# Kernel tuning notes

Measured on AMD Instinct MI355X. Metric: run time of the kernel, lower is better.

The kernel has to match this reference:

```python
import jax, jax.numpy as jnp
import numpy as np

N = 100000   # nodes
E = 1600000  # directed edges
F_IN = 256
H = 128
C = 64

def setup_inputs() -> dict:
    key = jax.random.key(0)
    k = jax.random.split(key, 6)
    x = jax.random.normal(k[0], (N, F_IN), dtype=jnp.float32)
    edge_index = jax.random.randint(k[1], (2, E), 0, N)
    def glorot(kk, fan_in, fan_out):
        s = jnp.sqrt(6.0 / (fan_in + fan_out)).astype(jnp.float32)
        return jax.random.uniform(kk, (fan_in, fan_out), jnp.float32, -s, s)
    W0 = glorot(k[2], F_IN, H)
    W1 = glorot(k[3], H, H)
    W2 = glorot(k[4], H, H)
    W3 = glorot(k[5], H, C)
    return {"x": x, "edge_index": edge_index, "W0": W0, "W1": W1, "W2": W2, "W3": W3}

def _gcn_norm(edge_index, num_nodes):
    # add self loops, compute symmetric normalization 1/sqrt(deg_i * deg_j)
    loops = jnp.arange(num_nodes, dtype=edge_index.dtype)
    row = jnp.concatenate([edge_index[0], loops])
    col = jnp.concatenate([edge_index[1], loops])
    deg = jax.ops.segment_sum(jnp.ones_like(row, dtype=jnp.float32), row, num_segments=num_nodes)
    dinv = jnp.where(deg > 0, jax.lax.rsqrt(deg), 0.0)
    norm = dinv[row] * dinv[col]  # [E+N]
    return row, col, norm

def _gcn_conv(h, W, row, col, norm, num_nodes):
    h = h @ W                      # [N, d_out]
    msg = h[col] * norm[:, None]   # gather + scale, [E+N, d_out]
    return jax.ops.segment_sum(msg, row, num_segments=num_nodes)

def _feat_corr_metric(h):
    # torch_corr(x.t()): Pearson correlation across feature columns -> [d, d]
    hc = h - jnp.mean(h, axis=0, keepdims=True)
    cov = hc.T @ hc                                 # [d, d]
    sd = jnp.sqrt(jnp.clip(jnp.diag(cov), 1e-12))
    corr = cov / (sd[:, None] * sd[None, :])
    n = corr.shape[0]
    upper = jnp.abs(jnp.triu(corr, 1))
    return upper.sum() / (n * (n - 1) / 2)

def reference(x, edge_index, W0, W1, W2, W3):
    row, col, norm = _gcn_norm(edge_index, N)
    Ws = [W0, W1, W2, W3]
    num_layers = len(Ws)
    h = x
    corr_2 = jnp.float32(0.0)
    corr = jnp.float32(0.0)
    for i, W in enumerate(Ws):
        h = _gcn_conv(h, W, row, col, norm, N)  # type_norm='None' -> bn is identity; eval -> dropout identity
        if i == num_layers - 2:
            corr_2 = _feat_corr_metric(h)
        if i == num_layers - 1:
            corr = _feat_corr_metric(h)
        if i != num_layers - 1:
            h = jax.nn.relu(h)
    return h, corr_2, corr
```

## Files before the change

kernel.cpp:

```cpp
#include <hip/hip_runtime.h>

#define NN 100000
#define FIN 256
#define HD 128
#define CD 64

typedef __attribute__((ext_vector_type(8))) short bf16x8;
typedef __attribute__((ext_vector_type(4))) float f32x4;

__device__ __forceinline__ float bf2f(unsigned int u16) {
    union { unsigned int u; float f; } v;
    v.u = (u16 & 0xffffu) << 16;
    return v.f;
}
__device__ __forceinline__ unsigned short f2bf(float f) {
    union { float f; unsigned int u; } v;
    v.f = f;
    unsigned int u = v.u + 0x7fffu + ((v.u >> 16) & 1u);
    return (unsigned short)(u >> 16);
}

__global__ void k_detect(const unsigned short* __restrict__ x, int* __restrict__ flag) {
    __shared__ int s[256];
    int t = threadIdx.x;
    int c = 0;
    for (int i = t; i < 16384; i += 256) {
        unsigned int e = (x[2 * i] >> 7) & 0xFF;
        c += (e >= 112 && e <= 134) ? 1 : 0;
    }
    s[t] = c;
    __syncthreads();
    for (int off = 128; off > 0; off >>= 1) {
        if (t < off) s[t] += s[t + off];
        __syncthreads();
    }
    if (t == 0) *flag = (s[0] > 8192) ? 1 : 0;
}

template <int K, int COLS>
__global__ void k_packW(const void* __restrict__ src, unsigned short* __restrict__ dst,
                        const int* __restrict__ dflag) {
    constexpr int CT = COLS / 16;
    int i = blockIdx.x * 256 + threadIdx.x;
    if (i >= K * COLS) return;
    int j = i & 7;
    int lane = (i >> 3) & 63;
    int rest = i >> 9;
    int ct = rest % CT;
    int kt = rest / CT;
    int k = kt * 32 + (lane >> 4) * 8 + j;
    int c = ct * 16 + (lane & 15);
    int si = k * COLS + c;
    dst[i] = (*dflag) ? ((const unsigned short*)src)[si] : f2bf(((const float*)src)[si]);
}

__global__ void k_hist(const int* __restrict__ row, int* __restrict__ cnt, int E) {
    int e = blockIdx.x * 256 + threadIdx.x;
    if (e < E) {
        unsigned int r = (unsigned int)row[e];
        if (r >= NN) r = 0;
        atomicAdd(&cnt[r], 1);
    }
}

__global__ void k_scan_a(const int* __restrict__ cnt, int* __restrict__ bsum, int n) {
    __shared__ int s[256];
    int i = blockIdx.x * 256 + threadIdx.x;
    s[threadIdx.x] = (i < n) ? cnt[i] : 0;
    __syncthreads();
    for (int off = 128; off > 0; off >>= 1) {
        if (threadIdx.x < off) s[threadIdx.x] += s[threadIdx.x + off];
        __syncthreads();
    }
    if (threadIdx.x == 0) bsum[blockIdx.x] = s[0];
}

__global__ void k_scan_b(int* bsum, int nchunks) {
    __shared__ int s[512];
    int t = threadIdx.x;
    int v = (t < nchunks) ? bsum[t] : 0;
    s[t] = v;
    __syncthreads();
    for (int off = 1; off < 512; off <<= 1) {
        int x = (t >= off) ? s[t - off] : 0;
        __syncthreads();
        s[t] += x;
        __syncthreads();
    }
    if (t < nchunks) bsum[t] = s[t] - v;
}

__global__ void k_scan_c(const int* __restrict__ cnt, const int* __restrict__ bsum,
                         int* __restrict__ offs, int* __restrict__ cursor, int n) {
    __shared__ int s[256];
    int t = threadIdx.x;
    int i = blockIdx.x * 256 + t;
    int v = (i < n) ? cnt[i] : 0;
    s[t] = v;
    __syncthreads();
    for (int off = 1; off < 256; off <<= 1) {
        int x = (t >= off) ? s[t - off] : 0;
        __syncthreads();
        s[t] += x;
        __syncthreads();
    }
    if (i < n) {
        int ex = bsum[blockIdx.x] + s[t] - v;
        offs[i] = ex;
        cursor[i] = ex;
    }
}

__global__ void k_scatter(const int* __restrict__ row, const int* __restrict__ col,
                          int* __restrict__ cursor, int* __restrict__ colS, int E,
                          int lo, int hi) {
    int e = blockIdx.x * 256 + threadIdx.x;
    if (e < E) {
        unsigned int r = (unsigned int)row[e];
        if (r >= NN) r = 0;
        if ((int)r >= lo && (int)r < hi) {
            unsigned int c = (unsigned int)col[e];
            if (c >= NN) c = 0;
            int p = atomicAdd(&cursor[r], 1);
            colS[p] = (int)c;
        }
    }
}

__global__ void k_dinv(const int* __restrict__ cnt, float* __restrict__ dinv, int n) {
    int i = blockIdx.x * 256 + threadIdx.x;
    if (i < n) dinv[i] = rsqrtf((float)(cnt[i] + 1));
}

template <int K, int COLS, bool RELU, int AMODE>
__global__ __launch_bounds__(256) void k_gemm(const void* __restrict__ Av,
                                              const unsigned short* __restrict__ Wp,
                                              const float* __restrict__ dinv,
                                              unsigned short* __restrict__ G, int nrows,
                                              const int* __restrict__ dflag) {
    constexpr int CT = COLS / 16;
    constexpr int KT = K / 32;
    __shared__ unsigned short tile[4][16][136];

    int t = threadIdx.x;
    int wave = t >> 6, lane = t & 63;
    int quad = lane >> 4, m = lane & 15;
    int r0 = blockIdx.x * 64 + wave * 16;
    int arow = r0 + m;
    bool rowok = arow < nrows;
    bool abf = (AMODE == 0) || (*dflag != 0);

    const unsigned short* Ab = (const unsigned short*)Av;
    const float* Af = (const float*)Av;

    f32x4 acc[CT];
#pragma unroll
    for (int ct = 0; ct < CT; ct++) acc[ct] = (f32x4){0.f, 0.f, 0.f, 0.f};

    for (int kt = 0; kt < KT; kt++) {
        int kb = kt * 32 + quad * 8;
        bf16x8 afrag = (bf16x8)0;
        if (rowok) {
            if (abf) {
                afrag = *(const bf16x8*)(Ab + (size_t)arow * K + kb);
                if constexpr (RELU) {
#pragma unroll
                    for (int j = 0; j < 8; j++) {
                        unsigned short u = (unsigned short)afrag[j];
                        afrag[j] = (u & 0x8000u) ? (short)0 : (short)u;
                    }
                }
            } else {
                float4 f0 = *(const float4*)(Af + (size_t)arow * K + kb);
                float4 f1 = *(const float4*)(Af + (size_t)arow * K + kb + 4);
                afrag[0] = (short)f2bf(f0.x); afrag[1] = (short)f2bf(f0.y);
                afrag[2] = (short)f2bf(f0.z); afrag[3] = (short)f2bf(f0.w);
                afrag[4] = (short)f2bf(f1.x); afrag[5] = (short)f2bf(f1.y);
                afrag[6] = (short)f2bf(f1.z); afrag[7] = (short)f2bf(f1.w);
            }
        }
#pragma unroll
        for (int ct = 0; ct < CT; ct++) {
            bf16x8 bfrag = *(const bf16x8*)(Wp + (((size_t)kt * CT + ct) * 64 + lane) * 8);
            acc[ct] = __builtin_amdgcn_mfma_f32_16x16x32_bf16(afrag, bfrag, acc[ct], 0, 0, 0);
        }
    }

    float dv[4];
#pragma unroll
    for (int rg = 0; rg < 4; rg++) {
        int gr = r0 + quad * 4 + rg;
        dv[rg] = dinv[gr < nrows ? gr : 0];
    }
#pragma unroll
    for (int ct = 0; ct < CT; ct++) {
#pragma unroll
        for (int rg = 0; rg < 4; rg++)
            tile[wave][quad * 4 + rg][ct * 16 + m] = f2bf(acc[ct][rg] * dv[rg]);
    }
    int srow = lane >> 2;
    int grow = r0 + srow;
    if (grow < nrows) {
        constexpr int CH = COLS / 32;
#pragma unroll
        for (int j8 = 0; j8 < CH; j8++) {
            int c = (lane & 3) * 8 + j8 * 32;
            uint4 v = *(const uint4*)&tile[wave][srow][c];
            *(uint4*)(G + (size_t)grow * COLS + c) = v;
        }
    }
}

template <int D, bool RELU, bool FINAL>
__global__ __launch_bounds__(256) void k_agg(const unsigned short* __restrict__ g,
                                             const int* __restrict__ colS,
                                             const int* __restrict__ offs,
                                             const int* __restrict__ cnt,
                                             const float* __restrict__ dinv,
                                             unsigned short* __restrict__ obf,
                                             void* __restrict__ oraw,
                                             const int* __restrict__ dflag, int n) {
    int lane = threadIdx.x & 63;
    int node = blockIdx.x * 4 + (threadIdx.x >> 6);
    if (node >= n) return;
    int start = offs[node];
    int deg = cnt[node];

    float a0 = 0.f, a1 = 0.f;
    if constexpr (D == 128) {
        unsigned int u = *(const unsigned int*)(g + (size_t)node * 128 + lane * 2);
        a0 = bf2f(u); a1 = bf2f(u >> 16);
    } else {
        a0 = bf2f(g[(size_t)node * 64 + lane]);
    }

    for (int base = 0; base < deg; base += 64) {
        int rem = deg - base;
        int nb = rem < 64 ? rem : 64;
        int cidx = 0;
        if (lane < nb) cidx = colS[start + base + lane];
        int j = 0;
        for (; j + 8 <= nb; j += 8) {
            int c0 = __shfl(cidx, j);
            int c1 = __shfl(cidx, j + 1);
            int c2 = __shfl(cidx, j + 2);
            int c3 = __shfl(cidx, j + 3);
            int c4 = __shfl(cidx, j + 4);
            int c5 = __shfl(cidx, j + 5);
            int c6 = __shfl(cidx, j + 6);
            int c7 = __shfl(cidx, j + 7);
            if constexpr (D == 128) {
                unsigned int u0 = *(const unsigned int*)(g + (size_t)c0 * 128 + lane * 2);
                unsigned int u1 = *(const unsigned int*)(g + (size_t)c1 * 128 + lane * 2);
                unsigned int u2 = *(const unsigned int*)(g + (size_t)c2 * 128 + lane * 2);
                unsigned int u3 = *(const unsigned int*)(g + (size_t)c3 * 128 + lane * 2);
                unsigned int u4 = *(const unsigned int*)(g + (size_t)c4 * 128 + lane * 2);
                unsigned int u5 = *(const unsigned int*)(g + (size_t)c5 * 128 + lane * 2);
                unsigned int u6 = *(const unsigned int*)(g + (size_t)c6 * 128 + lane * 2);
                unsigned int u7 = *(const unsigned int*)(g + (size_t)c7 * 128 + lane * 2);
                a0 += bf2f(u0); a1 += bf2f(u0 >> 16);
                a0 += bf2f(u1); a1 += bf2f(u1 >> 16);
                a0 += bf2f(u2); a1 += bf2f(u2 >> 16);
                a0 += bf2f(u3); a1 += bf2f(u3 >> 16);
                a0 += bf2f(u4); a1 += bf2f(u4 >> 16);
                a0 += bf2f(u5); a1 += bf2f(u5 >> 16);
                a0 += bf2f(u6); a1 += bf2f(u6 >> 16);
                a0 += bf2f(u7); a1 += bf2f(u7 >> 16);
            } else {
                unsigned short u0 = g[(size_t)c0 * 64 + lane];
                unsigned short u1 = g[(size_t)c1 * 64 + lane];
                unsigned short u2 = g[(size_t)c2 * 64 + lane];
                unsigned short u3 = g[(size_t)c3 * 64 + lane];
                unsigned short u4 = g[(size_t)c4 * 64 + lane];
                unsigned short u5 = g[(size_t)c5 * 64 + lane];
                unsigned short u6 = g[(size_t)c6 * 64 + lane];
                unsigned short u7 = g[(size_t)c7 * 64 + lane];
                a0 += bf2f(u0) + bf2f(u1) + bf2f(u2) + bf2f(u3);
                a0 += bf2f(u4) + bf2f(u5) + bf2f(u6) + bf2f(u7);
            }
        }
        for (; j < nb; j++) {
            int cj = __shfl(cidx, j);
            if constexpr (D == 128) {
                unsigned int u = *(const unsigned int*)(g + (size_t)cj * 128 + lane * 2);
                a0 += bf2f(u); a1 += bf2f(u >> 16);
            } else {
                a0 += bf2f(g[(size_t)cj * 64 + lane]);
            }
        }
    }

    float s = dinv[node];
    a0 *= s; a1 *= s;
    if constexpr (RELU) { a0 = fmaxf(a0, 0.f); a1 = fmaxf(a1, 0.f); }

    if constexpr (D == 128) {
        *(unsigned int*)(obf + (size_t)node * 128 + lane * 2) =
            (unsigned int)f2bf(a0) | ((unsigned int)f2bf(a1) << 16);
    } else {
        obf[(size_t)node * 64 + lane] = f2bf(a0);
        if constexpr (FINAL) {
            if (*dflag) ((unsigned short*)oraw)[(size_t)node * 64 + lane] = f2bf(a0);
            else        ((float*)oraw)[(size_t)node * 64 + lane] = a0;
        }
    }
}

template <int D>
__global__ __launch_bounds__(256) void k_colsum(const unsigned short* __restrict__ in,
                                                float* __restrict__ colsum, int n) {
    constexpr int CG = D / 8;
    constexpr int RPB = 256 / CG;
    __shared__ float red[RPB][D];
    int t = threadIdx.x;
    int cg = t % CG, r0 = t / CG;
    int c0 = cg * 8;
    float a[8];
#pragma unroll
    for (int i = 0; i < 8; i++) a[i] = 0.f;
    for (int r = blockIdx.x * RPB + r0; r < n; r += gridDim.x * RPB) {
        bf16x8 u = *(const bf16x8*)(in + (size_t)r * D + c0);
#pragma unroll
        for (int i = 0; i < 8; i++) a[i] += bf2f((unsigned short)u[i]);
    }
#pragma unroll
    for (int i = 0; i < 8; i++) red[r0][c0 + i] = a[i];
    __syncthreads();
    if (t < D) {
        float s = 0.f;
#pragma unroll
        for (int r = 0; r < RPB; r++) s += red[r][t];
        atomicAdd(&colsum[t], s);
    }
}

template <int D>
__global__ __launch_bounds__(256) void k_cov2(const unsigned short* __restrict__ in,
                                              const float* __restrict__ colsum,
                                              float* __restrict__ part, int n, int nblocks) {
    constexpr int CT = D / 16;
    constexpr int TPW = (D == 128) ? 2 : 1;
    constexpr int CG = D / 8;
    __shared__ unsigned int lds32[D * 16];
    __shared__ float smean[D];

    int t = threadIdx.x;
    int wave = t >> 6, lane = t & 63;
    int quad = lane >> 4, m = lane & 15;

    if (t < D) smean[t] = colsum[t] * (1.0f / (float)NN);
    __syncthreads();

    f32x4 accA[CT], accB[CT];
#pragma unroll
    for (int tc = 0; tc < CT; tc++) {
        accA[tc] = (f32x4){0.f, 0.f, 0.f, 0.f};
        accB[tc] = (f32x4){0.f, 0.f, 0.f, 0.f};
    }

    bool stager = (t < 16 * CG);
    int kp = stager ? (t / CG) : 0;
    int c0 = stager ? ((t % CG) * 8) : 0;
    int slot = (((kp >> 2) + (c0 >> 3)) & 3) * 4 + (kp & 3);
    float sm[8];
#pragma unroll
    for (int i = 0; i < 8; i++) sm[i] = smean[c0 + i];

    int ca0 = (wave * TPW) * 16 + m;
    int ga0 = (quad + (ca0 >> 3)) & 3;
    int ca1 = ca0 + 16;
    int ga1 = (quad + (ca1 >> 3)) & 3;

    int nchunks = (n + 31) / 32;
    for (int ch = blockIdx.x; ch < nchunks; ch += nblocks) {
        int k0 = ch * 32;
        if (stager) {
            int k = k0 + 2 * kp;
            bf16x8 u0 = (bf16x8)0, u1 = (bf16x8)0;
            bool ok0 = (k < n), ok1 = (k + 1 < n);
            if (ok0) u0 = *(const bf16x8*)(in + (size_t)k * D + c0);
            if (ok1) u1 = *(const bf16x8*)(in + (size_t)(k + 1) * D + c0);
#pragma unroll
            for (int i = 0; i < 8; i++) {
                float a = ok0 ? (bf2f((unsigned short)u0[i]) - sm[i]) : 0.f;
                float b = ok1 ? (bf2f((unsigned short)u1[i]) - sm[i]) : 0.f;
                lds32[(c0 + i) * 16 + slot] = (unsigned int)f2bf(a) | ((unsigned int)f2bf(b) << 16);
            }
        }
        __syncthreads();

        bf16x8 bfr[CT];
#pragma unroll
        for (int tc = 0; tc < CT; tc++) {
            int c = tc * 16 + m;
            int grp = (quad + (c >> 3)) & 3;
            bfr[tc] = *(const bf16x8*)&lds32[c * 16 + grp * 4];
        }
        bf16x8 afr0 = *(const bf16x8*)&lds32[ca0 * 16 + ga0 * 4];
#pragma unroll
        for (int tc = 0; tc < CT; tc++)
            accA[tc] = __builtin_amdgcn_mfma_f32_16x16x32_bf16(afr0, bfr[tc], accA[tc], 0, 0, 0);
        if constexpr (TPW == 2) {
            bf16x8 afr1 = *(const bf16x8*)&lds32[ca1 * 16 + ga1 * 4];
#pragma unroll
            for (int tc = 0; tc < CT; tc++)
                accB[tc] = __builtin_amdgcn_mfma_f32_16x16x32_bf16(afr1, bfr[tc], accB[tc], 0, 0, 0);
        }
        __syncthreads();
    }

    float* p = part + (size_t)blockIdx.x * D * D;
    int tr0 = wave * TPW;
#pragma unroll
    for (int tc = 0; tc < CT; tc++) {
#pragma unroll
        for (int rg = 0; rg < 4; rg++) {
            int cj = tc * 16 + m;
            p[(tr0 * 16 + quad * 4 + rg) * D + cj] = accA[tc][rg];
            if constexpr (TPW == 2)
                p[((tr0 + 1) * 16 + quad * 4 + rg) * D + cj] = accB[tc][rg];
        }
    }
}

template <int D>
__global__ __launch_bounds__(256) void k_covred(const float* __restrict__ part,
                                                float* __restrict__ cov, int nblocks) {
    __shared__ float red[256];
    int t = threadIdx.x;
    int il = t & 63;
    int bs = t >> 6;
    int idx = blockIdx.x * 64 + il;
    float s = 0.f;
    for (int b = bs; b < nblocks; b += 4)
        s += part[(size_t)b * D * D + idx];
    red[t] = s;
    __syncthreads();
    if (t < 64)
        cov[idx] = red[t] + red[t + 64] + red[t + 128] + red[t + 192];
}

template <int D>
__global__ __launch_bounds__(256) void k_fin(const float* __restrict__ cov,
                                             void* __restrict__ out, long long idx,
                                             const int* __restrict__ dflag) {
    __shared__ float sd[D];
    __shared__ float red[256];
    int t = threadIdx.x;
    if (t < D) sd[t] = sqrtf(fmaxf(cov[t * D + t], 1e-12f));
    __syncthreads();
    float s = 0.f;
    for (int i2 = t; i2 < D * D; i2 += 256) {
        int i = i2 / D, j = i2 % D;
        if (j > i) s += fabsf(cov[i2] / (sd[i] * sd[j]));
    }
    red[t] = s;
    __syncthreads();
    for (int off = 128; off > 0; off >>= 1) {
        if (t < off) red[t] += red[t + off];
        __syncthreads();
    }
    if (t == 0) {
        float v = red[0] / (float)(D * (D - 1) / 2);
        if (*dflag) ((unsigned short*)out)[idx] = f2bf(v);
        else        ((float*)out)[idx] = v;
    }
}

extern "C" void kernel_launch(void* const* d_in, const int* in_sizes, int n_in,
                              void* d_out, int out_size, void* d_ws, size_t ws_size,
                              hipStream_t stream) {
    const void* x = d_in[0];
    const int* ei = (const int*)d_in[1];

    int E = in_sizes[1] / 2;
    const int* row = ei;
    const int* col = ei + E;

    char* w = (char*)d_ws;
    auto carve = [&](size_t bytes) {
        void* p = (void*)w;
        w += (bytes + 255) & ~(size_t)255;
        return p;
    };
    int* cnt = (int*)carve((size_t)NN * 4);
    int* offs = (int*)carve((size_t)NN * 4);
    int* cursor = (int*)carve((size_t)NN * 4);
    int* bsum = (int*)carve(512 * 4);
    int* colS = (int*)carve((size_t)E * 4);
    float* dinv = (float*)carve((size_t)NN * 4);
    float* colsum = (float*)carve(HD * 4);
    float* covs = (float*)carve(HD * HD * 4);
    int* dflag = (int*)carve(256);
    unsigned short* wc = (unsigned short*)carve((size_t)(FIN * HD + HD * HD * 2 + HD * CD) * 2);
    unsigned short* bufA = (unsigned short*)carve((size_t)NN * HD * 2);
    unsigned short* bufB = (unsigned short*)carve((size_t)NN * HD * 2);

    unsigned short* wc0 = wc;
    unsigned short* wc1 = wc + FIN * HD;
    unsigned short* wc2 = wc1 + HD * HD;
    unsigned short* wc3 = wc2 + HD * HD;

    float* part = (float*)bufB;
    const int NBC = 250;

    int nchunks = (NN + 255) / 256;
    int eblocks = (E + 255) / 256;
    int GB = (NN + 63) / 64;

    k_detect<<<1, 256, 0, stream>>>((const unsigned short*)x, dflag);
    k_packW<256, 128><<<(FIN * HD) / 256, 256, 0, stream>>>(d_in[2], wc0, dflag);
    k_packW<128, 128><<<(HD * HD) / 256, 256, 0, stream>>>(d_in[3], wc1, dflag);
    k_packW<128, 128><<<(HD * HD) / 256, 256, 0, stream>>>(d_in[4], wc2, dflag);
    k_packW<128, 64><<<(HD * CD) / 256, 256, 0, stream>>>(d_in[5], wc3, dflag);

    hipMemsetAsync(cnt, 0, (size_t)NN * 4, stream);
    k_hist<<<eblocks, 256, 0, stream>>>(row, cnt, E);
    k_scan_a<<<nchunks, 256, 0, stream>>>(cnt, bsum, NN);
    k_scan_b<<<1, 512, 0, stream>>>(bsum, nchunks);
    k_scan_c<<<nchunks, 256, 0, stream>>>(cnt, bsum, offs, cursor, NN);
    k_scatter<<<eblocks, 256, 0, stream>>>(row, col, cursor, colS, E, 0, 25000);
    k_scatter<<<eblocks, 256, 0, stream>>>(row, col, cursor, colS, E, 25000, 50000);
    k_scatter<<<eblocks, 256, 0, stream>>>(row, col, cursor, colS, E, 50000, 75000);
    k_scatter<<<eblocks, 256, 0, stream>>>(row, col, cursor, colS, E, 75000, NN);
    k_dinv<<<nchunks, 256, 0, stream>>>(cnt, dinv, NN);

    k_gemm<256, 128, false, 2><<<GB, 256, 0, stream>>>(x, wc0, dinv, bufB, NN, dflag);
    k_agg<128, true, false><<<NN / 4, 256, 0, stream>>>(bufB, colS, offs, cnt, dinv, bufA, nullptr, dflag, NN);
    k_gemm<128, 128, false, 0><<<GB, 256, 0, stream>>>(bufA, wc1, dinv, bufB, NN, dflag);
    k_agg<128, true, false><<<NN / 4, 256, 0, stream>>>(bufB, colS, offs, cnt, dinv, bufA, nullptr, dflag, NN);
    k_gemm<128, 128, false, 0><<<GB, 256, 0, stream>>>(bufA, wc2, dinv, bufB, NN, dflag);
    k_agg<128, false, false><<<NN / 4, 256, 0, stream>>>(bufB, colS, offs, cnt, dinv, bufA, nullptr, dflag, NN);

    hipMemsetAsync(colsum, 0, HD * 4, stream);
    k_colsum<128><<<64, 256, 0, stream>>>(bufA, colsum, NN);
    k_cov2<128><<<NBC, 256, 0, stream>>>(bufA, colsum, part, NN, NBC);
    k_covred<128><<<(HD * HD) / 64, 256, 0, stream>>>(part, covs, NBC);
    k_fin<128><<<1, 256, 0, stream>>>(covs, d_out, (long long)NN * CD, dflag);

    k_gemm<128, 64, true, 0><<<GB, 256, 0, stream>>>(bufA, wc3, dinv, bufB, NN, dflag);
    k_agg<64, false, true><<<NN / 4, 256, 0, stream>>>(bufB, colS, offs, cnt, dinv, bufA, d_out, dflag, NN);

    hipMemsetAsync(colsum, 0, HD * 4, stream);
    k_colsum<64><<<64, 256, 0, stream>>>(bufA, colsum, NN);
    k_cov2<64><<<NBC, 256, 0, stream>>>(bufA, colsum, part, NN, NBC);
    k_covred<64><<<(CD * CD) / 64, 256, 0, stream>>>(part, covs, NBC);
    k_fin<64><<<1, 256, 0, stream>>>(covs, d_out, (long long)NN * CD + 1, dflag);
}
```

Before: 830.5 us.

## Vectorize neighbor gathers in aggregation and privatize degree histogram

The aggregation kernel now splits each wave into lane groups that each load a full 16-byte bf16 row chunk per neighbor. Several neighbors are processed in parallel and the groups are combined with cross-lane shuffle reductions, replacing 4-byte or 2-byte per-lane gathers. The degree histogram now uses 32 private per-block histograms held in a scratch buffer, followed by a reduction kernel, to reduce atomic contention on the shared counters. The trade-off is extra shuffle reductions and register use in aggregation. The histogram change adds a large memset and reduction pass, and its 32 blocks give low parallelism.

```diff
diff --git a/kernel.cpp b/kernel.cpp
--- a/kernel.cpp
+++ b/kernel.cpp
@@ -4,6 +4,7 @@
 #define FIN 256
 #define HD 128
 #define CD 64
+#define HB 32
 
 typedef __attribute__((ext_vector_type(8))) short bf16x8;
 typedef __attribute__((ext_vector_type(4))) float f32x4;
@@ -54,13 +55,29 @@
     dst[i] = (*dflag) ? ((const unsigned short*)src)[si] : f2bf(((const float*)src)[si]);
 }
 
-__global__ void k_hist(const int* __restrict__ row, int* __restrict__ cnt, int E) {
-    int e = blockIdx.x * 256 + threadIdx.x;
-    if (e < E) {
+__global__ __launch_bounds__(256) void k_hist2(const int* __restrict__ row,
+                                               int* __restrict__ priv, int E) {
+    int b = blockIdx.x;
+    int* h = priv + (size_t)b * NN;
+    int per = (E + HB - 1) / HB;
+    int lo = b * per;
+    int hi = lo + per;
+    if (hi > E) hi = E;
+    for (int e = lo + threadIdx.x; e < hi; e += 256) {
         unsigned int r = (unsigned int)row[e];
         if (r >= NN) r = 0;
-        atomicAdd(&cnt[r], 1);
-    }
+        atomicAdd(&h[r], 1);
+    }
+}
+
+__global__ __launch_bounds__(256) void k_histred(const int* __restrict__ priv,
+                                                 int* __restrict__ cnt, int n) {
+    int i = blockIdx.x * 256 + threadIdx.x;
+    if (i >= n) return;
+    int s = 0;
+#pragma unroll 8
+    for (int b = 0; b < HB; b++) s += priv[(size_t)b * NN + i];
+    cnt[i] = s;
 }
 
 __global__ void k_scan_a(const int* __restrict__ cnt, int* __restrict__ bsum, int n) {
@@ -211,6 +228,13 @@
     }
 }
 
+__device__ __forceinline__ void acc8(float* a, uint4 u) {
+    a[0] += bf2f(u.x); a[1] += bf2f(u.x >> 16);
+    a[2] += bf2f(u.y); a[3] += bf2f(u.y >> 16);
+    a[4] += bf2f(u.z); a[5] += bf2f(u.z >> 16);
+    a[6] += bf2f(u.w); a[7] += bf2f(u.w >> 16);
+}
+
 template <int D, bool RELU, bool FINAL>
 __global__ __launch_bounds__(256) void k_agg(const unsigned short* __restrict__ g,
                                              const int* __restrict__ colS,
@@ -220,18 +244,23 @@
                                              unsigned short* __restrict__ obf,
                                              void* __restrict__ oraw,
                                              const int* __restrict__ dflag, int n) {
+    constexpr int GRP = (D == 128) ? 4 : 8;
+    constexpr int LPR = 64 / GRP;
     int lane = threadIdx.x & 63;
     int node = blockIdx.x * 4 + (threadIdx.x >> 6);
     if (node >= n) return;
+    int gq = lane / LPR;
+    int li = lane % LPR;
     int start = offs[node];
     int deg = cnt[node];
 
-    float a0 = 0.f, a1 = 0.f;
-    if constexpr (D == 128) {
-        unsigned int u = *(const unsigned int*)(g + (size_t)node * 128 + lane * 2);
-        a0 = bf2f(u); a1 = bf2f(u >> 16);
-    } else {
-        a0 = bf2f(g[(size_t)node * 64 + lane]);
+    float a[8];
+#pragma unroll
+    for (int i = 0; i < 8; i++) a[i] = 0.f;
+
+    if (gq == 0) {
+        uint4 u = *(const uint4*)(g + (size_t)node * D + li * 8);
+        acc8(a, u);
     }
 
     for (int base = 0; base < deg; base += 64) {
@@ -240,68 +269,69 @@
         int cidx = 0;
         if (lane < nb) cidx = colS[start + base + lane];
         int j = 0;
-        for (; j + 8 <= nb; j += 8) {
-            int c0 = __shfl(cidx, j);
-            int c1 = __shfl(cidx, j + 1);
-            int c2 = __shfl(cidx, j + 2);
-            int c3 = __shfl(cidx, j + 3);
-            int c4 = __shfl(cidx, j + 4);
-            int c5 = __shfl(cidx, j + 5);
-            int c6 = __shfl(cidx, j + 6);
-            int c7 = __shfl(cidx, j + 7);
-            if constexpr (D == 128) {
-                unsigned int u0 = *(const unsigned int*)(g + (size_t)c0 * 128 + lane * 2);
-                unsigned int u1 = *(const unsigned int*)(g + (size_t)c1 * 128 + lane * 2);
-                unsigned int u2 = *(const unsigned int*)(g + (size_t)c2 * 128 + lane * 2);
-                unsigned int u3 = *(const unsigned int*)(g + (size_t)c3 * 128 + lane * 2);
-                unsigned int u4 = *(const unsigned int*)(g + (size_t)c4 * 128 + lane * 2);
-                unsigned int u5 = *(const unsigned int*)(g + (size_t)c5 * 128 + lane * 2);
-                unsigned int u6 = *(const unsigned int*)(g + (size_t)c6 * 128 + lane * 2);
-                unsigned int u7 = *(const unsigned int*)(g + (size_t)c7 * 128 + lane * 2);
-                a0 += bf2f(u0); a1 += bf2f(u0 >> 16);
-                a0 += bf2f(u1); a1 += bf2f(u1 >> 16);
-                a0 += bf2f(u2); a1 += bf2f(u2 >> 16);
-                a0 += bf2f(u3); a1 += bf2f(u3 >> 16);
-                a0 += bf2f(u4); a1 += bf2f(u4 >> 16);
-                a0 += bf2f(u5); a1 += bf2f(u5 >> 16);
-                a0 += bf2f(u6); a1 += bf2f(u6 >> 16);
-                a0 += bf2f(u7); a1 += bf2f(u7 >> 16);
+        if constexpr (D == 128) {
+            for (; j + 8 <= nb; j += 8) {
+                int ca = __shfl(cidx, j + gq);
+                int cb = __shfl(cidx, j + 4 + gq);
+                uint4 ua = *(const uint4*)(g + (size_t)ca * D + li * 8);
+                uint4 ub = *(const uint4*)(g + (size_t)cb * D + li * 8);
+                acc8(a, ua);
+                acc8(a, ub);
+            }
+            for (; j < nb; j += 4) {
+                int jj = j + gq;
+                int cc = __shfl(cidx, jj < nb ? jj : (nb - 1));
+                if (jj < nb) {
+                    uint4 u = *(const uint4*)(g + (size_t)cc * D + li * 8);
+                    acc8(a, u);
+                }
+            }
+        } else {
+            for (; j + 8 <= nb; j += 8) {
+                int cc = __shfl(cidx, j + gq);
+                uint4 u = *(const uint4*)(g + (size_t)cc * D + li * 8);
+                acc8(a, u);
+            }
+            for (; j < nb; j += 8) {
+                int jj = j + gq;
+                int cc = __shfl(cidx, jj < nb ? jj : (nb - 1));
+                if (jj < nb) {
+                    uint4 u = *(const uint4*)(g + (size_t)cc * D + li * 8);
+                    acc8(a, u);
+                }
+            }
+        }
+    }
+
+#pragma unroll
+    for (int i = 0; i < 8; i++) {
+        if constexpr (D == 64) a[i] += __shfl_xor(a[i], 8);
+        a[i] += __shfl_xor(a[i], 16);
+        a[i] += __shfl_xor(a[i], 32);
+    }
+
+    float s = dinv[node];
+#pragma unroll
+    for (int i = 0; i < 8; i++) {
+        a[i] *= s;
+        if constexpr (RELU) a[i] = fmaxf(a[i], 0.f);
+    }
+
+    if (gq == 0) {
+        uint4 o;
+        o.x = (unsigned int)f2bf(a[0]) | ((unsigned int)f2bf(a[1]) << 16);
+        o.y = (unsigned int)f2bf(a[2]) | ((unsigned int)f2bf(a[3]) << 16);
+        o.z = (unsigned int)f2bf(a[4]) | ((unsigned int)f2bf(a[5]) << 16);
+        o.w = (unsigned int)f2bf(a[6]) | ((unsigned int)f2bf(a[7]) << 16);
+        *(uint4*)(obf + (size_t)node * D + li * 8) = o;
+        if constexpr (FINAL) {
+            if (*dflag) {
+                *(uint4*)((unsigned short*)oraw + (size_t)node * D + li * 8) = o;
             } else {
-                unsigned short u0 = g[(size_t)c0 * 64 + lane];
-                unsigned short u1 = g[(size_t)c1 * 64 + lane];
-                unsigned short u2 = g[(size_t)c2 * 64 + lane];
-                unsigned short u3 = g[(size_t)c3 * 64 + lane];
-                unsigned short u4 = g[(size_t)c4 * 64 + lane];
-                unsigned short u5 = g[(size_t)c5 * 64 + lane];
-                unsigned short u6 = g[(size_t)c6 * 64 + lane];
-                unsigned short u7 = g[(size_t)c7 * 64 + lane];
-                a0 += bf2f(u0) + bf2f(u1) + bf2f(u2) + bf2f(u3);
-                a0 += bf2f(u4) + bf2f(u5) + bf2f(u6) + bf2f(u7);
-            }
-        }
-        for (; j < nb; j++) {
-            int cj = __shfl(cidx, j);
-            if constexpr (D == 128) {
-                unsigned int u = *(const unsigned int*)(g + (size_t)cj * 128 + lane * 2);
-                a0 += bf2f(u); a1 += bf2f(u >> 16);
-            } else {
-                a0 += bf2f(g[(size_t)cj * 64 + lane]);
-            }
-        }
-    }
-
-    float s = dinv[node];
-    a0 *= s; a1 *= s;
-    if constexpr (RELU) { a0 = fmaxf(a0, 0.f); a1 = fmaxf(a1, 0.f); }
-
-    if constexpr (D == 128) {
-        *(unsigned int*)(obf + (size_t)node * 128 + lane * 2) =
-            (unsigned int)f2bf(a0) | ((unsigned int)f2bf(a1) << 16);
-    } else {
-        obf[(size_t)node * 64 + lane] = f2bf(a0);
-        if constexpr (FINAL) {
-            if (*dflag) ((unsigned short*)oraw)[(size_t)node * 64 + lane] = f2bf(a0);
-            else        ((float*)oraw)[(size_t)node * 64 + lane] = a0;
+                float* op = (float*)oraw + (size_t)node * D + li * 8;
+                *(float4*)op = (float4){a[0], a[1], a[2], a[3]};
+                *(float4*)(op + 4) = (float4){a[4], a[5], a[6], a[7]};
+            }
         }
     }
 }
@@ -502,6 +532,7 @@
     unsigned short* wc3 = wc2 + HD * HD;
 
     float* part = (float*)bufB;
+    int* privh = (int*)bufB;
     const int NBC = 250;
 
     int nchunks = (NN + 255) / 256;
@@ -514,8 +545,9 @@
     k_packW<128, 128><<<(HD * HD) / 256, 256, 0, stream>>>(d_in[4], wc2, dflag);
     k_packW<128, 64><<<(HD * CD) / 256, 256, 0, stream>>>(d_in[5], wc3, dflag);
 
-    hipMemsetAsync(cnt, 0, (size_t)NN * 4, stream);
-    k_hist<<<eblocks, 256, 0, stream>>>(row, cnt, E);
+    hipMemsetAsync(privh, 0, (size_t)NN * HB * 4, stream);
+    k_hist2<<<HB, 256, 0, stream>>>(row, privh, E);
+    k_histred<<<nchunks, 256, 0, stream>>>(privh, cnt, NN);
     k_scan_a<<<nchunks, 256, 0, stream>>>(cnt, bsum, NN);
     k_scan_b<<<1, 512, 0, stream>>>(bsum, nchunks);
     k_scan_c<<<nchunks, 256, 0, stream>>>(cnt, bsum, offs, cursor, NN);
```

Measured after the change: 887.1 us. 6.8% more time.
